# Kernel optimization log

Measured on AMD Instinct MI355X. Metric: run time of the kernel, lower is better.

Reference implementation:

```python
import jax, jax.numpy as jnp
import numpy as np

UNITS = 512
IN_DIM = 256


def setup_inputs() -> dict:
    key = jax.random.key(0)
    k1, k2, k3 = jax.random.split(key, 3)
    x = jax.random.normal(k1, (128, 512, IN_DIM), dtype=jnp.float32)
    # glorot_uniform for kernel
    lim = float(np.sqrt(6.0 / (IN_DIM + UNITS)))
    kernel = jax.random.uniform(k2, (IN_DIM, UNITS), minval=-lim, maxval=lim, dtype=jnp.float32)
    # orthogonal init for recurrent kernel
    a = jax.random.normal(k3, (UNITS, UNITS), dtype=jnp.float32)
    q, r = jnp.linalg.qr(a)
    recurrent_kernel = q * jnp.sign(jnp.diag(r))[None, :]
    bias = jnp.zeros((UNITS,), dtype=jnp.float32)
    return {"x": x, "kernel": kernel, "recurrent_kernel": recurrent_kernel, "bias": bias}


def reference(x, kernel, recurrent_kernel, bias):
    # h_t = tanh(x_t @ W_x + b + h_{t-1} @ W_h), return full sequence [B, T, U]
    B = x.shape[0]
    # Precompute input projection for all timesteps in one batched GEMM
    xp = jnp.einsum('btf,fu->btu', x, kernel) + bias  # [B, T, U]

    def step(h, xp_t):
        h_new = jnp.tanh(xp_t + h @ recurrent_kernel)
        return h_new, h_new

    h0 = jnp.zeros((B, UNITS), dtype=x.dtype)
    _, ys = jax.lax.scan(step, h0, jnp.swapaxes(xp, 0, 1))  # ys: [T, B, U]
    return jnp.swapaxes(ys, 0, 1)
```

## Files before the change

kernel.cpp:

```cpp
#include <hip/hip_runtime.h>
#include <math.h>


#define BM 64
#define BN 64
#define BK 32
#define SENT 0xFFFFFFFFu

__global__ __launch_bounds__(256) void xp_gemm(
    const float* __restrict__ x,
    const float* __restrict__ wx,
    const float* __restrict__ bias,
    float* __restrict__ xp)
{
    __shared__ float As[BK][BM + 4];
    __shared__ float Bs[BK][BN + 4];

    const int tid = threadIdx.x;
    const int m0 = blockIdx.y * BM;
    const int n0 = blockIdx.x * BN;
    const int tm = tid / 16;
    const int tn = tid % 16;

    float acc[4][4] = {};

    for (int k0 = 0; k0 < 256; k0 += BK) {
        {
            const int kk = tid % BK;
            const int r0 = tid / BK;
            #pragma unroll
            for (int rr = 0; rr < 8; ++rr) {
                const int m = r0 + rr * 8;
                As[kk][m] = x[(size_t)(m0 + m) * 256 + (k0 + kk)];
            }
        }
        {
            const int nn = tid % BN;
            const int r0 = tid / BN;
            #pragma unroll
            for (int rr = 0; rr < 8; ++rr) {
                const int k = r0 + rr * 4;
                Bs[k][nn] = wx[(size_t)(k0 + k) * 512 + (n0 + nn)];
            }
        }
        __syncthreads();

        #pragma unroll
        for (int kk = 0; kk < BK; ++kk) {
            const float4 a = *(const float4*)&As[kk][tm * 4];
            const float4 b = *(const float4*)&Bs[kk][tn * 4];
            const float av[4] = {a.x, a.y, a.z, a.w};
            const float bv[4] = {b.x, b.y, b.z, b.w};
            #pragma unroll
            for (int i = 0; i < 4; ++i)
                #pragma unroll
                for (int j = 0; j < 4; ++j)
                    acc[i][j] += av[i] * bv[j];
        }
        __syncthreads();
    }

    #pragma unroll
    for (int i = 0; i < 4; ++i) {
        const int m = m0 + tm * 4 + i;
        #pragma unroll
        for (int j = 0; j < 4; ++j) {
            const int n = n0 + tn * 4 + j;
            xp[(size_t)m * 512 + n] = acc[i][j] + bias[n];
        }
    }
}

#define FMA4(A, W, H) { (A).x += (H)*(W).x; (A).y += (H)*(W).y; (A).z += (H)*(W).z; (A).w += (H)*(W).w; }
#define PIN4(W) asm volatile("" : "+v"((W).x), "+v"((W).y), "+v"((W).z), "+v"((W).w))

__global__ __launch_bounds__(1024, 4) void rnn_scan4(
    const float* __restrict__ wh,
    const float* __restrict__ xp,
    float* __restrict__ out)
{
    __shared__ float h_lds[2][512];
    __shared__ float red[32][2][128];

    const int tid = threadIdx.x;
    const int us  = blockIdx.x & 3;
    const int bg  = blockIdx.x >> 2;
    const int u0  = us * 128;
    const int g   = tid & 31;
    const int s   = tid >> 5;
    const int kbase = s * 16;
    const size_t seq = 512 * 512;

    const float* wr = &wh[(size_t)kbase * 512 + (u0 + 4 * g)];
    float4 w0  = *(const float4*)(wr + 0  * 512);
    float4 w1  = *(const float4*)(wr + 1  * 512);
    float4 w2  = *(const float4*)(wr + 2  * 512);
    float4 w3  = *(const float4*)(wr + 3  * 512);
    float4 w4  = *(const float4*)(wr + 4  * 512);
    float4 w5  = *(const float4*)(wr + 5  * 512);
    float4 w6  = *(const float4*)(wr + 6  * 512);
    float4 w7  = *(const float4*)(wr + 7  * 512);
    float4 w8  = *(const float4*)(wr + 8  * 512);
    float4 w9  = *(const float4*)(wr + 9  * 512);
    float4 w10 = *(const float4*)(wr + 10 * 512);
    float4 w11 = *(const float4*)(wr + 11 * 512);
    float4 w12 = *(const float4*)(wr + 12 * 512);
    float4 w13 = *(const float4*)(wr + 13 * 512);
    float4 w14 = *(const float4*)(wr + 14 * 512);
    float4 w15 = *(const float4*)(wr + 15 * 512);
    PIN4(w0);  PIN4(w1);  PIN4(w2);  PIN4(w3);
    PIN4(w4);  PIN4(w5);  PIN4(w6);  PIN4(w7);
    PIN4(w8);  PIN4(w9);  PIN4(w10); PIN4(w11);
    PIN4(w12); PIN4(w13); PIN4(w14); PIN4(w15);

    const int ru = tid & 127;
    const int rb = (tid >> 7) & 1;
    const float* xpp = xp + (size_t)(bg * 2 + rb) * seq + u0 + ru;
    float*       hop = out + (size_t)(bg * 2 + rb) * seq + u0 + ru;

    const int sb   = (tid >= 384) ? 1 : 0;
    const int srem = tid - sb * 384;
    const int shk  = (srem < u0) ? srem : srem + 128;
    const float* pollp = out + (size_t)(bg * 2 + sb) * seq + shk;

    for (int t = 0; t < 512; ++t) {
        float xpv = 0.0f;
        if (tid < 256) xpv = xpp[(size_t)t * 512];

        if (t == 0) {
            ((float*)h_lds)[tid] = 0.0f;
        } else if (tid < 768) {
            const float* p = pollp + (size_t)(t - 1) * 512;
            float v;
            int cnt = 0;
            do {
                v = __hip_atomic_load(p, __ATOMIC_RELAXED, __HIP_MEMORY_SCOPE_AGENT);
                if (__float_as_uint(v) != SENT) break;
                __builtin_amdgcn_s_sleep(1);
            } while (++cnt < (1 << 20));
            h_lds[sb][shk] = v;
        }
        __syncthreads();

        float4 a0 = make_float4(0.f, 0.f, 0.f, 0.f);
        float4 a1 = make_float4(0.f, 0.f, 0.f, 0.f);
        const float* hb0 = &h_lds[0][kbase];
        const float* hb1 = &h_lds[1][kbase];
        #define STEP4(W0, W1, W2, W3, OFF) { \
            const float4 h0 = *(const float4*)(hb0 + (OFF)); \
            const float4 h1 = *(const float4*)(hb1 + (OFF)); \
            FMA4(a0, W0, h0.x) FMA4(a0, W1, h0.y) FMA4(a0, W2, h0.z) FMA4(a0, W3, h0.w) \
            FMA4(a1, W0, h1.x) FMA4(a1, W1, h1.y) FMA4(a1, W2, h1.z) FMA4(a1, W3, h1.w) }
        STEP4(w0,  w1,  w2,  w3,  0)
        STEP4(w4,  w5,  w6,  w7,  4)
        STEP4(w8,  w9,  w10, w11, 8)
        STEP4(w12, w13, w14, w15, 12)
        #undef STEP4

        *(float4*)&red[s][0][4 * g] = a0;
        *(float4*)&red[s][1][4 * g] = a1;
        __syncthreads();

        if (tid < 256) {
            float r = xpv;
            #pragma unroll
            for (int ss = 0; ss < 32; ++ss) r += red[ss][rb][ru];
            const float hn = tanhf(r);
            h_lds[rb][u0 + ru] = hn;
            __hip_atomic_store(hop + (size_t)t * 512, hn,
                               __ATOMIC_RELAXED, __HIP_MEMORY_SCOPE_AGENT);
        }
        __syncthreads();
    }
}

__global__ __launch_bounds__(1024) void rnn_scan3(
    const float* __restrict__ wh, float* __restrict__ out, int* __restrict__ flags)
{
    __shared__ float smem[21504];
    float* h_lds = smem;
    float* red   = smem + 1024;

    const int tid = threadIdx.x;
    const int us  = blockIdx.x & 3;
    const int bg  = blockIdx.x >> 2;
    const int u0  = us * 128;
    const int g   = tid & 31;
    const int s   = tid >> 5;
    const int kbase = s * 16;

    float4 w[16];
    #pragma unroll
    for (int i = 0; i < 16; ++i)
        w[i] = *(const float4*)&wh[(size_t)(kbase + i) * 512 + (u0 + 4 * g)];

    float* out0 = out + (size_t)(bg * 2 + 0) * (512 * 512);
    float* out1 = out + (size_t)(bg * 2 + 1) * (512 * 512);
    const int ru = tid & 127;
    const int rb = tid >> 7;
    int* myflag = flags + bg * 512;

    for (int t = 0; t < 512; ++t) {
        float xpv = 0.f;
        if (tid < 256) {
            const float* op = (rb == 0) ? out0 : out1;
            xpv = op[(size_t)t * 512 + u0 + ru];
        }
        if (t == 0) {
            h_lds[tid] = 0.f;
        } else {
            if (tid == 0) {
                int v, cnt = 0;
                do {
                    v = __hip_atomic_load(&myflag[t - 1], __ATOMIC_RELAXED, __HIP_MEMORY_SCOPE_AGENT);
                    if (v < 4) __builtin_amdgcn_s_sleep(2);
                } while (v < 4 && ++cnt < (1 << 22));
                (void)__hip_atomic_load(&myflag[t - 1], __ATOMIC_ACQUIRE, __HIP_MEMORY_SCOPE_AGENT);
            }
            __syncthreads();
            const int hb = tid >> 9;
            const int hk = tid & 511;
            const float* src = ((hb == 0) ? out0 : out1) + (size_t)(t - 1) * 512 + hk;
            h_lds[hb * 512 + hk] = __hip_atomic_load(src, __ATOMIC_RELAXED, __HIP_MEMORY_SCOPE_AGENT);
        }
        __syncthreads();

        float4 a0 = make_float4(0.f, 0.f, 0.f, 0.f);
        float4 a1 = make_float4(0.f, 0.f, 0.f, 0.f);
        #pragma unroll
        for (int i = 0; i < 4; ++i) {
            const float4 h0 = *(const float4*)&h_lds[0 * 512 + kbase + 4 * i];
            const float4 h1 = *(const float4*)&h_lds[1 * 512 + kbase + 4 * i];
            FMA4(a0, w[4*i+0], h0.x) FMA4(a0, w[4*i+1], h0.y) FMA4(a0, w[4*i+2], h0.z) FMA4(a0, w[4*i+3], h0.w)
            FMA4(a1, w[4*i+0], h1.x) FMA4(a1, w[4*i+1], h1.y) FMA4(a1, w[4*i+2], h1.z) FMA4(a1, w[4*i+3], h1.w)
        }
        *(float4*)&red[(s * 2 + 0) * 128 + 4 * g] = a0;
        *(float4*)&red[(s * 2 + 1) * 128 + 4 * g] = a1;
        __syncthreads();

        if (tid < 256) {
            float r = xpv;
            #pragma unroll
            for (int ss = 0; ss < 32; ++ss) r += red[(ss * 2 + rb) * 128 + ru];
            const float hn = tanhf(r);
            float* op = (rb == 0) ? out0 : out1;
            __hip_atomic_store(&op[(size_t)t * 512 + u0 + ru], hn,
                               __ATOMIC_RELAXED, __HIP_MEMORY_SCOPE_AGENT);
        }
        __syncthreads();
        if (tid == 0)
            __hip_atomic_fetch_add(&myflag[t], 1, __ATOMIC_RELEASE, __HIP_MEMORY_SCOPE_AGENT);
    }
}

__global__ __launch_bounds__(1024, 4) void rnn_scan2(
    const float* __restrict__ wh, float* __restrict__ out)
{
    __shared__ float h_lds[2][512];
    __shared__ float red[8][2][512];

    const int tid = threadIdx.x;
    const int g = tid & 127;
    const int s = tid >> 7;
    const int b = tid >> 9;
    const int u = tid & 511;

    float* seqb = out + (size_t)(2 * blockIdx.x + b) * 512 * 512;
    h_lds[b][u] = 0.0f;
    __syncthreads();

    const float4* __restrict__ whv = (const float4*)wh;
    const int kbase = s * 64;

    for (int t = 0; t < 512; ++t) {
        const float xpv = seqb[(size_t)t * 512 + u];
        float4 a0 = make_float4(0.f, 0.f, 0.f, 0.f);
        float4 a1 = make_float4(0.f, 0.f, 0.f, 0.f);
        #pragma unroll 4
        for (int kk = 0; kk < 64; kk += 4) {
            const int k = kbase + kk;
            const float4 h0 = *(const float4*)&h_lds[0][k];
            const float4 h1 = *(const float4*)&h_lds[1][k];
            const float4 v0 = whv[(k + 0) * 128 + g];
            const float4 v1 = whv[(k + 1) * 128 + g];
            const float4 v2 = whv[(k + 2) * 128 + g];
            const float4 v3 = whv[(k + 3) * 128 + g];
            FMA4(a0, v0, h0.x) FMA4(a0, v1, h0.y) FMA4(a0, v2, h0.z) FMA4(a0, v3, h0.w)
            FMA4(a1, v0, h1.x) FMA4(a1, v1, h1.y) FMA4(a1, v2, h1.z) FMA4(a1, v3, h1.w)
        }
        *(float4*)&red[s][0][4 * g] = a0;
        *(float4*)&red[s][1][4 * g] = a1;
        __syncthreads();
        float r = xpv;
        #pragma unroll
        for (int ss = 0; ss < 8; ++ss) r += red[ss][b][u];
        const float hn = tanhf(r);
        h_lds[b][u] = hn;
        seqb[(size_t)t * 512 + u] = hn;
        __syncthreads();
    }
}

extern "C" void kernel_launch(void* const* d_in, const int* in_sizes, int n_in,
                              void* d_out, int out_size, void* d_ws, size_t ws_size,
                              hipStream_t stream) {
    const float* x    = (const float*)d_in[0];
    const float* wx   = (const float*)d_in[1];
    const float* wh   = (const float*)d_in[2];
    const float* bias = (const float*)d_in[3];
    float* out = (float*)d_out;

    dim3 g1(512 / BN, 65536 / BM);
    const size_t xp_bytes = (size_t)128 * 512 * 512 * sizeof(float);
    const size_t flag_bytes = 64 * 512 * sizeof(int);

    if (d_ws != nullptr && ws_size >= xp_bytes) {
        hipMemsetAsync(d_out, 0xFF, xp_bytes, stream);
        xp_gemm<<<g1, 256, 0, stream>>>(x, wx, bias, (float*)d_ws);
        rnn_scan4<<<256, 1024, 0, stream>>>(wh, (const float*)d_ws, out);
    } else if (d_ws != nullptr && ws_size >= flag_bytes) {
        hipMemsetAsync(d_ws, 0, flag_bytes, stream);
        xp_gemm<<<g1, 256, 0, stream>>>(x, wx, bias, out);
        rnn_scan3<<<256, 1024, 0, stream>>>(wh, out, (int*)d_ws);
    } else {
        xp_gemm<<<g1, 256, 0, stream>>>(x, wx, bias, out);
        rnn_scan2<<<64, 1024, 0, stream>>>(wh, out);
    }
}
```

Measured before the change: 1.276 ms.

## Poll hidden state directly per-thread and drop LDS broadcast barrier in RNN scan

Each thread now reads its own 16-element slice of the previous hidden state straight from global memory with relaxed atomic loads, retrying only entries that still hold the sentinel. This removes the LDS staging of h and the barrier after polling, and the first half of the FMAs starts before the second half has arrived. Block-to-(unit slice, batch group) mapping is transposed so blocks sharing a batch are spread apart, and step 0 is peeled to skip the zero-state matmul. It adds many more global polling loads per step and redundant reads of the same h values across warps, which raises cache traffic.

```diff
diff --git a/kernel.cpp b/kernel.cpp
--- a/kernel.cpp
+++ b/kernel.cpp
@@ -6,6 +6,8 @@
 #define BN 64
 #define BK 32
 #define SENT 0xFFFFFFFFu
+#define AL(p) __hip_atomic_load((p), __ATOMIC_RELAXED, __HIP_MEMORY_SCOPE_AGENT)
+#define AS(p, v) __hip_atomic_store((p), (v), __ATOMIC_RELAXED, __HIP_MEMORY_SCOPE_AGENT)
 
 __global__ __launch_bounds__(256) void xp_gemm(
     const float* __restrict__ x,
@@ -74,17 +76,16 @@
 #define FMA4(A, W, H) { (A).x += (H)*(W).x; (A).y += (H)*(W).y; (A).z += (H)*(W).z; (A).w += (H)*(W).w; }
 #define PIN4(W) asm volatile("" : "+v"((W).x), "+v"((W).y), "+v"((W).z), "+v"((W).w))
 
-__global__ __launch_bounds__(1024, 4) void rnn_scan4(
+__global__ __launch_bounds__(1024, 4) void rnn_scan5(
     const float* __restrict__ wh,
     const float* __restrict__ xp,
     float* __restrict__ out)
 {
-    __shared__ float h_lds[2][512];
     __shared__ float red[32][2][128];
 
     const int tid = threadIdx.x;
-    const int us  = blockIdx.x & 3;
-    const int bg  = blockIdx.x >> 2;
+    const int us  = blockIdx.x >> 6;
+    const int bg  = blockIdx.x & 63;
     const int u0  = us * 128;
     const int g   = tid & 31;
     const int s   = tid >> 5;
@@ -118,44 +119,70 @@
     const float* xpp = xp + (size_t)(bg * 2 + rb) * seq + u0 + ru;
     float*       hop = out + (size_t)(bg * 2 + rb) * seq + u0 + ru;
 
-    const int sb   = (tid >= 384) ? 1 : 0;
-    const int srem = tid - sb * 384;
-    const int shk  = (srem < u0) ? srem : srem + 128;
-    const float* pollp = out + (size_t)(bg * 2 + sb) * seq + shk;
-
-    for (int t = 0; t < 512; ++t) {
+    const float* h0base = out + (size_t)(bg * 2 + 0) * seq + kbase;
+    const float* h1base = out + (size_t)(bg * 2 + 1) * seq + kbase;
+
+    if (tid < 256) {
+        AS(hop, tanhf(xpp[0]));
+    }
+
+    for (int t = 1; t < 512; ++t) {
         float xpv = 0.0f;
         if (tid < 256) xpv = xpp[(size_t)t * 512];
 
-        if (t == 0) {
-            ((float*)h_lds)[tid] = 0.0f;
-        } else if (tid < 768) {
-            const float* p = pollp + (size_t)(t - 1) * 512;
-            float v;
-            int cnt = 0;
-            do {
-                v = __hip_atomic_load(p, __ATOMIC_RELAXED, __HIP_MEMORY_SCOPE_AGENT);
-                if (__float_as_uint(v) != SENT) break;
-                __builtin_amdgcn_s_sleep(1);
-            } while (++cnt < (1 << 20));
-            h_lds[sb][shk] = v;
-        }
-        __syncthreads();
+        const float* s0 = h0base + (size_t)(t - 1) * 512;
+        const float* s1 = h1base + (size_t)(t - 1) * 512;
+
+        float hA0[8], hA1[8], hB0[8], hB1[8];
+        #pragma unroll
+        for (int i = 0; i < 8; ++i) hA0[i] = AL(s0 + i);
+        #pragma unroll
+        for (int i = 0; i < 8; ++i) hA1[i] = AL(s1 + i);
+        #pragma unroll
+        for (int i = 0; i < 8; ++i) hB0[i] = AL(s0 + 8 + i);
+        #pragma unroll
+        for (int i = 0; i < 8; ++i) hB1[i] = AL(s1 + 8 + i);
 
         float4 a0 = make_float4(0.f, 0.f, 0.f, 0.f);
         float4 a1 = make_float4(0.f, 0.f, 0.f, 0.f);
-        const float* hb0 = &h_lds[0][kbase];
-        const float* hb1 = &h_lds[1][kbase];
-        #define STEP4(W0, W1, W2, W3, OFF) { \
-            const float4 h0 = *(const float4*)(hb0 + (OFF)); \
-            const float4 h1 = *(const float4*)(hb1 + (OFF)); \
-            FMA4(a0, W0, h0.x) FMA4(a0, W1, h0.y) FMA4(a0, W2, h0.z) FMA4(a0, W3, h0.w) \
-            FMA4(a1, W0, h1.x) FMA4(a1, W1, h1.y) FMA4(a1, W2, h1.z) FMA4(a1, W3, h1.w) }
-        STEP4(w0,  w1,  w2,  w3,  0)
-        STEP4(w4,  w5,  w6,  w7,  4)
-        STEP4(w8,  w9,  w10, w11, 8)
-        STEP4(w12, w13, w14, w15, 12)
-        #undef STEP4
+
+        for (int pass = 0; pass < (1 << 20); ++pass) {
+            unsigned bad = 0;
+            #pragma unroll
+            for (int i = 0; i < 8; ++i)
+                bad |= (unsigned)(__float_as_uint(hA0[i]) == SENT)
+                     | (unsigned)(__float_as_uint(hA1[i]) == SENT);
+            if (!bad) break;
+            if (pass > 4) __builtin_amdgcn_s_sleep(1);
+            #pragma unroll
+            for (int i = 0; i < 8; ++i) {
+                if (__float_as_uint(hA0[i]) == SENT) hA0[i] = AL(s0 + i);
+                if (__float_as_uint(hA1[i]) == SENT) hA1[i] = AL(s1 + i);
+            }
+        }
+        FMA4(a0, w0, hA0[0]) FMA4(a0, w1, hA0[1]) FMA4(a0, w2, hA0[2]) FMA4(a0, w3, hA0[3])
+        FMA4(a0, w4, hA0[4]) FMA4(a0, w5, hA0[5]) FMA4(a0, w6, hA0[6]) FMA4(a0, w7, hA0[7])
+        FMA4(a1, w0, hA1[0]) FMA4(a1, w1, hA1[1]) FMA4(a1, w2, hA1[2]) FMA4(a1, w3, hA1[3])
+        FMA4(a1, w4, hA1[4]) FMA4(a1, w5, hA1[5]) FMA4(a1, w6, hA1[6]) FMA4(a1, w7, hA1[7])
+
+        for (int pass = 0; pass < (1 << 20); ++pass) {
+            unsigned bad = 0;
+            #pragma unroll
+            for (int i = 0; i < 8; ++i)
+                bad |= (unsigned)(__float_as_uint(hB0[i]) == SENT)
+                     | (unsigned)(__float_as_uint(hB1[i]) == SENT);
+            if (!bad) break;
+            if (pass > 4) __builtin_amdgcn_s_sleep(1);
+            #pragma unroll
+            for (int i = 0; i < 8; ++i) {
+                if (__float_as_uint(hB0[i]) == SENT) hB0[i] = AL(s0 + 8 + i);
+                if (__float_as_uint(hB1[i]) == SENT) hB1[i] = AL(s1 + 8 + i);
+            }
+        }
+        FMA4(a0, w8,  hB0[0]) FMA4(a0, w9,  hB0[1]) FMA4(a0, w10, hB0[2]) FMA4(a0, w11, hB0[3])
+        FMA4(a0, w12, hB0[4]) FMA4(a0, w13, hB0[5]) FMA4(a0, w14, hB0[6]) FMA4(a0, w15, hB0[7])
+        FMA4(a1, w8,  hB1[0]) FMA4(a1, w9,  hB1[1]) FMA4(a1, w10, hB1[2]) FMA4(a1, w11, hB1[3])
+        FMA4(a1, w12, hB1[4]) FMA4(a1, w13, hB1[5]) FMA4(a1, w14, hB1[6]) FMA4(a1, w15, hB1[7])
 
         *(float4*)&red[s][0][4 * g] = a0;
         *(float4*)&red[s][1][4 * g] = a1;
@@ -166,9 +193,7 @@
             #pragma unroll
             for (int ss = 0; ss < 32; ++ss) r += red[ss][rb][ru];
             const float hn = tanhf(r);
-            h_lds[rb][u0 + ru] = hn;
-            __hip_atomic_store(hop + (size_t)t * 512, hn,
-                               __ATOMIC_RELAXED, __HIP_MEMORY_SCOPE_AGENT);
+            AS(hop + (size_t)t * 512, hn);
         }
         __syncthreads();
     }
@@ -317,7 +342,7 @@
     if (d_ws != nullptr && ws_size >= xp_bytes) {
         hipMemsetAsync(d_out, 0xFF, xp_bytes, stream);
         xp_gemm<<<g1, 256, 0, stream>>>(x, wx, bias, (float*)d_ws);
-        rnn_scan4<<<256, 1024, 0, stream>>>(wh, (const float*)d_ws, out);
+        rnn_scan5<<<256, 1024, 0, stream>>>(wh, (const float*)d_ws, out);
     } else if (d_ws != nullptr && ws_size >= flag_bytes) {
         hipMemsetAsync(d_ws, 0, flag_bytes, stream);
         xp_gemm<<<g1, 256, 0, stream>>>(x, wx, bias, out);
```

New measurement: 1.799 ms. 41.0% more time.
